# Performance work log

Measured on AMD Instinct MI355X. Metric: run time of the kernel, lower is better.

Reference implementation:

```python
import jax, jax.numpy as jnp
import numpy as np
from math import factorial

B, C, D = 1024, 10, 16
EPS = 1e-07


def _moment_weights(dim, order):
    # weight[idx] = prod(multiplicity!)/order!  (de-duplicates symmetric index tuples)
    if order == 1:
        return np.ones((dim,), dtype=np.float32)
    grids = np.meshgrid(*([np.arange(dim)] * order), indexing='ij')
    idx = np.stack(grids, axis=-1)  # [dim]*order + [order]
    prodm = np.ones(idx.shape[:-1], dtype=np.float64)
    for p in range(order):
        r = np.ones(idx.shape[:-1], dtype=np.float64)
        for q in range(p):
            r += (idx[..., q] == idx[..., p])
        prodm *= r  # running multiplicities multiply to prod(m!)
    return (prodm / float(factorial(order))).astype(np.float32)


def _gauss_moments(dim, order):
    # joint moments of N(0, I) via Isserlis' theorem
    eye = np.eye(dim)
    if order == 1:
        return np.zeros((dim,), np.float32)
    if order == 2:
        return eye.astype(np.float32)
    if order == 3:
        return np.zeros((dim, dim, dim), np.float32)
    g = (np.einsum('ij,kl->ijkl', eye, eye)
         + np.einsum('ik,jl->ijkl', eye, eye)
         + np.einsum('il,jk->ijkl', eye, eye))
    return g.astype(np.float32)


def _sroot(x, c1, p, c2):
    # signed compressive root: sign(sign(x)+0.1) * ((|x|+c1)^p - c2)
    return jnp.sign(jnp.sign(x) + 0.1) * (jnp.power(jnp.abs(x) + c1, p) - c2)


def setup_inputs() -> dict:
    key = jax.random.key(0)
    k1, k2, k3 = jax.random.split(key, 3)
    return {
        'embedding': jax.random.normal(k1, (B, D), dtype=jnp.float32),
        'centers': jax.random.normal(k2, (C, D), dtype=jnp.float32),
        'logits': jax.random.normal(k3, (B, C), dtype=jnp.float32),
        'gm1': jnp.asarray(_gauss_moments(D, 1)),
        'gm2': jnp.asarray(_gauss_moments(D, 2)),
        'gm3': jnp.asarray(_gauss_moments(D, 3)),
        'gm4': jnp.asarray(_gauss_moments(D, 4)),
        'mw1': jnp.asarray(_moment_weights(D, 1)),
        'mw2': jnp.asarray(_moment_weights(D, 2)),
        'mw3': jnp.asarray(_moment_weights(D, 3)),
        'mw4': jnp.asarray(_moment_weights(D, 4)),
    }


def reference(embedding, centers, logits, gm1, gm2, gm3, gm4, mw1, mw2, mw3, mw4):
    num_classes = logits.shape[1]
    assign = jnp.argmax(logits, axis=-1)                      # [B]
    onehot = jax.nn.one_hot(assign, num_classes, dtype=embedding.dtype)  # [B,C]
    diff = embedding[:, None, :] - centers[None, :, :]        # [B,C,D]
    d = diff * onehot[:, :, None]                             # diff_onehot [B,C,D]
    cw = jnp.sum(onehot, axis=0)                              # cluster_weight [C]

    # fused moment contractions (original materializes [B,C,D^k] then sums over B;
    # onehot is 0/1 so onehot^k == onehot -> identical math)
    m1 = jnp.sum(d, axis=0) / (cw[:, None] + EPS)                             # [C,D]
    m2 = jnp.einsum('bci,bcj->cij', d, d) / (cw[:, None, None] + EPS)         # [C,D,D]
    m3 = jnp.einsum('bci,bcj,bck->cijk', d, d, d)                             # [C,D,D,D] (no count division, as in original)
    m4 = jnp.einsum('bci,bcj,bck,bcl->cijkl', d, d, d, d)                     # [C,D,D,D,D]

    m2 = _sroot(m2, 0.25, 0.5, 0.5)
    m3 = _sroot(m3, 0.19245008973, 0.3333333333, 0.57735026919)
    m4 = _sroot(m4, 0.15749013123, 0.25, 0.62996052494)
    t1 = gm1
    t2 = _sroot(gm2, 0.25, 0.5, 0.5)
    t3 = _sroot(gm3, 0.19245008973, 0.3333333333, 0.57735026919)
    t4 = _sroot(gm4, 0.15749013123, 0.25, 0.62996052494)

    cwn = cw / jnp.sum(cw)                                     # [C]
    w1 = cwn[:, None] * mw1[None, :]
    w2 = cwn[:, None, None] * mw2[None]
    w3 = cwn[:, None, None, None] * mw3[None]
    w4 = cwn[:, None, None, None, None] * mw4[None]

    p1 = jnp.sum(w1 * jnp.square(m1 - t1[None]))
    p2 = jnp.sum(w2 * jnp.square(m2 - t2[None]))
    p3 = jnp.sum(w3 * jnp.square(m3 - t3[None]))
    p4 = jnp.sum(w4 * jnp.square(m4 - t4[None]))
    return 1.0 * p1 + 0.5 * p2 + 0.25 * p3 + 0.125 * p4
```

## Files before the change

kernel.cpp:

```cpp
#include <hip/hip_runtime.h>
#include <math.h>

#define BN 1024
#define CN 10
#define DN 16
#define NE1 16
#define NE2 136
#define NE3 816
#define NE4 3876
#define NENT 4844
#define EB 19
#define CH 256
#define SST 260
#define EPSV 1e-7f

__device__ __forceinline__ int H2f(int n){ return n*(n+1)/2; }
__device__ __forceinline__ int H3f(int n){ return n*(n+1)*(n+2)/6; }

__device__ __forceinline__ float sroot2f(float x){
  float s = (x<0.f)?-1.f:1.f;
  return s*(sqrtf(fabsf(x)+0.25f)-0.5f);
}
__device__ __forceinline__ float sroot3f(float x){
  float s=(x<0.f)?-1.f:1.f;
  return s*(cbrtf(fabsf(x)+0.19245008973f)-0.57735026919f);
}
__device__ __forceinline__ float sroot4f(float x){
  float s=(x<0.f)?-1.f:1.f;
  return s*(sqrtf(sqrtf(fabsf(x)+0.15749013123f))-0.62996052494f);
}

__global__ __launch_bounds__(256) void kb(
    const float* __restrict__ emb, const float* __restrict__ centers,
    const float* __restrict__ logits,
    const float* __restrict__ gm1, const float* __restrict__ gm2,
    const float* __restrict__ gm3, const float* __restrict__ gm4,
    float* __restrict__ out) {
  __shared__ float sx[DN][SST];
  __shared__ int   memb[BN];
  __shared__ int   wcnt[4][4];
  __shared__ float wred[4];
  int tid  = threadIdx.x;
  int lane = tid & 63;
  int wave = tid >> 6;
  int c  = blockIdx.x / EB;
  int eb = blockIdx.x % EB;

  int rank_r[4]; bool match_r[4];
  #pragma unroll
  for (int r=0;r<4;r++) {
    int b = r*256 + tid;
    const float* lr = logits + b*CN;
    float best = lr[0]; int bi = 0;
    #pragma unroll
    for (int q=1;q<CN;q++){ float v=lr[q]; if (v>best){best=v;bi=q;} }
    unsigned long long m = __ballot(bi==c);
    match_r[r] = (bi==c);
    rank_r[r] = __popcll(m & ((1ull<<lane)-1ull));
    if (lane==0) wcnt[r][wave] = __popcll(m);
  }

  int e = eb*256 + tid;
  int ii=0, jj=0, kk=0, ll=0, order=0;
  float tg = 0.f;
  bool valid = (e < NENT);
  if (valid) {
    if (e < NE1) {
      order=1; ii=e;
      tg = gm1[ii];
    } else if (e < NE1+NE2) {
      order=2; int r = e-NE1;
      int i=0; while (r >= DN-i){ r -= DN-i; i++; }
      ii=i; jj=i+r;
      tg = sroot2f(gm2[ii*DN+jj]);
    } else if (e < NE1+NE2+NE3) {
      order=3; int r = e-(NE1+NE2);
      int i=0; while (r >= H2f(DN-i)){ r -= H2f(DN-i); i++; }
      int j=i; while (r >= DN-j){ r -= DN-j; j++; }
      ii=i; jj=j; kk=j+r;
      tg = sroot3f(gm3[(ii*DN+jj)*DN+kk]);
    } else {
      order=4; int r = e-(NE1+NE2+NE3);
      int i=0; while (r >= H3f(DN-i)){ r -= H3f(DN-i); i++; }
      int j=i; while (r >= H2f(DN-j)){ r -= H2f(DN-j); j++; }
      int k=j; while (r >= DN-k){ r -= DN-k; k++; }
      ii=i; jj=j; kk=k; ll=k+r;
      tg = sroot4f(gm4[((ii*DN+jj)*DN+kk)*DN+ll]);
    }
  }

  __syncthreads();
  int pre[17]; pre[0]=0;
  #pragma unroll
  for (int p=0;p<16;p++) pre[p+1] = pre[p] + wcnt[p>>2][p&3];
  int cnt = pre[16];
  #pragma unroll
  for (int r=0;r<4;r++)
    if (match_r[r]) memb[pre[r*4+wave] + rank_r[r]] = r*256 + tid;

  const float* pA = &sx[ii][0];
  const float* pB = &sx[jj][0];
  const float* pC = &sx[kk][0];
  const float* pD = &sx[ll][0];

  float mom = 0.f;
  for (int base=0; base<cnt; base+=CH) {
    int m  = min(CH, cnt-base);
    int mp = (m+3)&~3;
    __syncthreads();
    if (tid < m) {
      int b = memb[base + tid];
      const float4* er = (const float4*)(emb + b*DN);
      const float4* cr = (const float4*)(centers + c*DN);
      float4 e0=er[0], e1=er[1], e2=er[2], e3=er[3];
      float4 c0=cr[0], c1=cr[1], c2=cr[2], c3=cr[3];
      float v[16];
      v[0]=e0.x-c0.x; v[1]=e0.y-c0.y; v[2]=e0.z-c0.z; v[3]=e0.w-c0.w;
      v[4]=e1.x-c1.x; v[5]=e1.y-c1.y; v[6]=e1.z-c1.z; v[7]=e1.w-c1.w;
      v[8]=e2.x-c2.x; v[9]=e2.y-c2.y; v[10]=e2.z-c2.z; v[11]=e2.w-c2.w;
      v[12]=e3.x-c3.x; v[13]=e3.y-c3.y; v[14]=e3.z-c3.z; v[15]=e3.w-c3.w;
      #pragma unroll
      for (int i=0;i<DN;i++) sx[i][tid] = v[i];
    }
    if (tid < DN)
      for (int n=m; n<mp; n++) sx[tid][n] = 0.f;
    __syncthreads();
    if (order==4) {
      for (int n=0; n<mp; n+=4) {
        float4 a=*(const float4*)(pA+n), b=*(const float4*)(pB+n);
        float4 cc=*(const float4*)(pC+n), d=*(const float4*)(pD+n);
        mom += a.x*b.x*cc.x*d.x + a.y*b.y*cc.y*d.y
             + a.z*b.z*cc.z*d.z + a.w*b.w*cc.w*d.w;
      }
    } else if (order==3) {
      for (int n=0; n<mp; n+=4) {
        float4 a=*(const float4*)(pA+n), b=*(const float4*)(pB+n);
        float4 cc=*(const float4*)(pC+n);
        mom += a.x*b.x*cc.x + a.y*b.y*cc.y + a.z*b.z*cc.z + a.w*b.w*cc.w;
      }
    } else if (order==2) {
      for (int n=0; n<mp; n+=4) {
        float4 a=*(const float4*)(pA+n), b=*(const float4*)(pB+n);
        mom += a.x*b.x + a.y*b.y + a.z*b.z + a.w*b.w;
      }
    } else if (order==1) {
      for (int n=0; n<mp; n+=4) {
        float4 a=*(const float4*)(pA+n);
        mom += a.x + a.y + a.z + a.w;
      }
    }
  }

  float contrib = 0.f;
  if (valid) {
    float mval = mom;
    if (order <= 2) mval /= ((float)cnt + EPSV);
    float v;
    if      (order==1) v = mval - tg;
    else if (order==2) v = sroot2f(mval) - tg;
    else if (order==3) v = sroot3f(mval) - tg;
    else               v = sroot4f(mval) - tg;
    float lw = (order==1)?1.f:(order==2)?0.5f:(order==3)?0.25f:0.125f;
    float cwn = (float)cnt * (1.f/1024.f);
    contrib = lw * cwn * v * v;
  }

  #pragma unroll
  for (int off=32; off; off>>=1) contrib += __shfl_down(contrib, off, 64);
  if (lane==0) wred[wave] = contrib;
  __syncthreads();
  if (tid==0) atomicAdd(out, wred[0]+wred[1]+wred[2]+wred[3]);
}

extern "C" void kernel_launch(void* const* d_in, const int* in_sizes, int n_in,
                              void* d_out, int out_size, void* d_ws, size_t ws_size,
                              hipStream_t stream) {
  const float* emb  = (const float*)d_in[0];
  const float* cen  = (const float*)d_in[1];
  const float* logi = (const float*)d_in[2];
  const float* gm1  = (const float*)d_in[3];
  const float* gm2  = (const float*)d_in[4];
  const float* gm3  = (const float*)d_in[5];
  const float* gm4  = (const float*)d_in[6];

  hipMemsetAsync(d_out, 0, sizeof(float), stream);
  kb<<<CN*EB, 256, 0, stream>>>(emb, cen, logi, gm1, gm2, gm3, gm4, (float*)d_out);
}
```

Baseline: 18.11 us.

## Precompute pairwise products in shared memory to cut per-entry moment reads

Adds a shared-memory table Q of all 136 pairwise products d_i*d_j per sample, filled cooperatively by the four waves (34 pairs each), so order-3 and order-4 moment entries read two operands instead of three or four. Order-2 entries read a single precomputed product. The chunk size drops to 88 samples so that Q fits in LDS, which adds chunk iterations and barriers. Logits are also loaded as float2 pairs. Shared memory use grows substantially, which may limit occupancy.

```diff
diff --git a/kernel.cpp b/kernel.cpp
--- a/kernel.cpp
+++ b/kernel.cpp
@@ -4,18 +4,20 @@
 #define BN 1024
 #define CN 10
 #define DN 16
+#define NP2 136
 #define NE1 16
 #define NE2 136
 #define NE3 816
 #define NE4 3876
 #define NENT 4844
 #define EB 19
-#define CH 256
-#define SST 260
+#define CH 88
+#define SST 92
 #define EPSV 1e-7f
 
 __device__ __forceinline__ int H2f(int n){ return n*(n+1)/2; }
 __device__ __forceinline__ int H3f(int n){ return n*(n+1)*(n+2)/6; }
+__device__ __forceinline__ int rank2(int i,int j){ return i*DN - (i*(i-1))/2 + (j-i); }
 
 __device__ __forceinline__ float sroot2f(float x){
   float s = (x<0.f)?-1.f:1.f;
@@ -37,6 +39,7 @@
     const float* __restrict__ gm3, const float* __restrict__ gm4,
     float* __restrict__ out) {
   __shared__ float sx[DN][SST];
+  __shared__ float Q[NP2][SST];
   __shared__ int   memb[BN];
   __shared__ int   wcnt[4][4];
   __shared__ float wred[4];
@@ -50,10 +53,12 @@
   #pragma unroll
   for (int r=0;r<4;r++) {
     int b = r*256 + tid;
-    const float* lr = logits + b*CN;
-    float best = lr[0]; int bi = 0;
+    const float2* l2 = (const float2*)(logits + b*CN);
+    float2 q0=l2[0], q1=l2[1], q2=l2[2], q3=l2[3], q4=l2[4];
+    float vv[10] = {q0.x,q0.y,q1.x,q1.y,q2.x,q2.y,q3.x,q3.y,q4.x,q4.y};
+    float best = vv[0]; int bi = 0;
     #pragma unroll
-    for (int q=1;q<CN;q++){ float v=lr[q]; if (v>best){best=v;bi=q;} }
+    for (int q=1;q<CN;q++){ if (vv[q]>best){best=vv[q];bi=q;} }
     unsigned long long m = __ballot(bi==c);
     match_r[r] = (bi==c);
     rank_r[r] = __popcll(m & ((1ull<<lane)-1ull));
@@ -89,6 +94,13 @@
     }
   }
 
+  const float* PA = &sx[0][0];
+  const float* PB = &sx[0][0];
+  if (order==1)      PA = &sx[ii][0];
+  else if (order==2) PA = &Q[rank2(ii,jj)][0];
+  else if (order==3) { PA = &Q[rank2(ii,jj)][0]; PB = &sx[kk][0]; }
+  else if (order==4) { PA = &Q[rank2(ii,jj)][0]; PB = &Q[rank2(kk,ll)][0]; }
+
   __syncthreads();
   int pre[17]; pre[0]=0;
   #pragma unroll
@@ -98,10 +110,9 @@
   for (int r=0;r<4;r++)
     if (match_r[r]) memb[pre[r*4+wave] + rank_r[r]] = r*256 + tid;
 
-  const float* pA = &sx[ii][0];
-  const float* pB = &sx[jj][0];
-  const float* pC = &sx[kk][0];
-  const float* pD = &sx[ll][0];
+  int qp0 = 34*wave;
+  int qi=0, qrem=qp0; while (qrem >= DN-qi){ qrem -= DN-qi; qi++; }
+  int qj0 = qi + qrem;
 
   float mom = 0.f;
   for (int base=0; base<cnt; base+=CH) {
@@ -125,27 +136,26 @@
     if (tid < DN)
       for (int n=m; n<mp; n++) sx[tid][n] = 0.f;
     __syncthreads();
-    if (order==4) {
+    for (int n0=lane; n0<mp; n0+=64) {
+      float v[DN];
+      #pragma unroll
+      for (int i=0;i<DN;i++) v[i] = sx[i][n0];
+      int pi=qi, pj=qj0;
+      #pragma unroll
+      for (int t=0;t<34;t++) {
+        Q[qp0+t][n0] = v[pi]*v[pj];
+        pj++; if (pj==DN){ pi++; pj=pi; }
+      }
+    }
+    __syncthreads();
+    if (order>=3) {
       for (int n=0; n<mp; n+=4) {
-        float4 a=*(const float4*)(pA+n), b=*(const float4*)(pB+n);
-        float4 cc=*(const float4*)(pC+n), d=*(const float4*)(pD+n);
-        mom += a.x*b.x*cc.x*d.x + a.y*b.y*cc.y*d.y
-             + a.z*b.z*cc.z*d.z + a.w*b.w*cc.w*d.w;
-      }
-    } else if (order==3) {
-      for (int n=0; n<mp; n+=4) {
-        float4 a=*(const float4*)(pA+n), b=*(const float4*)(pB+n);
-        float4 cc=*(const float4*)(pC+n);
-        mom += a.x*b.x*cc.x + a.y*b.y*cc.y + a.z*b.z*cc.z + a.w*b.w*cc.w;
-      }
-    } else if (order==2) {
-      for (int n=0; n<mp; n+=4) {
-        float4 a=*(const float4*)(pA+n), b=*(const float4*)(pB+n);
+        float4 a=*(const float4*)(PA+n), b=*(const float4*)(PB+n);
         mom += a.x*b.x + a.y*b.y + a.z*b.z + a.w*b.w;
       }
-    } else if (order==1) {
+    } else if (order>=1) {
       for (int n=0; n<mp; n+=4) {
-        float4 a=*(const float4*)(pA+n);
+        float4 a=*(const float4*)(PA+n);
         mom += a.x + a.y + a.z + a.w;
       }
     }
```

Measured after the change: 32.10 us. 1.77x slower.
